# Optimization experiments

Hardware: AMD Instinct MI355X
Metric: run time of the kernel (lower is better)

Reference implementation:

```python
import jax, jax.numpy as jnp
import numpy as np

N = 50000      # nodes
E = 800000     # edges (avg degree 16)
CIN = 64       # in_channels
COUT = 128     # hidden_channels (block out_channels)
TC = 512       # time_channels = 4*hidden
H = 4          # attention heads
DH = COUT // H # head dim
G = 8          # group-norm groups
SLOPE = 0.01   # LeakyReLU default slope


def group_norm(x, w, b, groups=G, eps=1e-5):
    n, c = x.shape
    xg = x.reshape(n, groups, c // groups)
    mu = xg.mean(-1, keepdims=True)
    var = xg.var(-1, keepdims=True)
    xn = ((xg - mu) * jax.lax.rsqrt(var + eps)).reshape(n, c)
    return xn * w + b


def gcn_conv(x, W, b, row, col, ew, n):
    # GCNConv: add self loops (weight 1), symmetric normalization
    sl = jnp.arange(n)
    r = jnp.concatenate([row, sl])
    c = jnp.concatenate([col, sl])
    w2 = jnp.concatenate([ew, jnp.ones((n,), ew.dtype)])
    deg = jax.ops.segment_sum(w2, c, num_segments=n)
    dinv = jnp.where(deg > 0, jax.lax.rsqrt(deg), 0.0)
    norm = dinv[r] * w2 * dinv[c]            # [E+N]
    xw = x @ W                                # [N, Cout]
    out = jax.ops.segment_sum(norm[:, None] * xw[r], c, num_segments=n)
    return out + b


def gat_conv(x, Wa, a_src, a_dst, a_edge, ba, row, col, ew, n):
    # GAT-style attention conv; self-loop edge weight filled with max(edge_weight)
    sl = jnp.arange(n)
    fill = ew.max()
    r = jnp.concatenate([row, sl])
    c = jnp.concatenate([col, sl])
    w2 = jnp.concatenate([ew, jnp.full((n,), fill, ew.dtype)])
    h = (x @ Wa).reshape(n, H, DH)            # [N, H, DH]
    al_s = (h * a_src).sum(-1)                # [N, H]
    al_d = (h * a_dst).sum(-1)                # [N, H]
    logits = jax.nn.leaky_relu(al_s[r] + al_d[c] + a_edge * w2[:, None], 0.2)
    m = jax.ops.segment_max(logits, c, num_segments=n)
    e = jnp.exp(logits - m[c])
    s = jax.ops.segment_sum(e, c, num_segments=n)
    alpha = e / (s[c] + 1e-16)                # [E+N, H]
    out = jax.ops.segment_sum(alpha[:, :, None] * h[r], c, num_segments=n)
    return out.reshape(n, H * DH) + ba


def setup_inputs() -> dict:
    key = jax.random.key(0)
    ks = jax.random.split(key, 24)
    def w(k, shape, fan_in):
        return (jax.random.normal(k, shape, jnp.float32) / np.sqrt(fan_in)).astype(jnp.float32)
    inp = {
        "x": jax.random.normal(ks[0], (N, CIN), jnp.float32),
        "t": jax.random.normal(ks[1], (TC,), jnp.float32),
        "edge_index": jax.random.randint(ks[2], (2, E), 0, N, jnp.int32),
        "edge_weight": jax.random.uniform(ks[3], (E,), jnp.float32),
        # ResBlock norm/conv params
        "gn0_w": jnp.ones((CIN,), jnp.float32), "gn0_b": jnp.zeros((CIN,), jnp.float32),
        "W1": w(ks[4], (CIN, COUT), CIN), "b1": jnp.zeros((COUT,), jnp.float32),
        "gn1_w": jnp.ones((COUT,), jnp.float32), "gn1_b": jnp.zeros((COUT,), jnp.float32),
        "W2": w(ks[5], (COUT, COUT), COUT), "b2": jnp.zeros((COUT,), jnp.float32),
        "Wres": w(ks[6], (CIN, COUT), CIN),
        "te_w": w(ks[7], (TC, COUT), TC), "te_b": jnp.zeros((COUT,), jnp.float32),
        # AttnBlock params
        "gn2_w": jnp.ones((COUT,), jnp.float32), "gn2_b": jnp.zeros((COUT,), jnp.float32),
        "Wa": w(ks[8], (COUT, H * DH), COUT),
        "a_src": w(ks[9], (H, DH), DH), "a_dst": w(ks[10], (H, DH), DH),
        "a_edge": w(ks[11], (H,), 1), "ba": jnp.zeros((H * DH,), jnp.float32),
    }
    return inp


def reference(x, t, edge_index, edge_weight,
              gn0_w, gn0_b, W1, b1, gn1_w, gn1_b, W2, b2, Wres, te_w, te_b,
              gn2_w, gn2_b, Wa, a_src, a_dst, a_edge, ba):
    row, col = edge_index[0], edge_index[1]
    leaky = lambda z: jax.nn.leaky_relu(z, SLOPE)
    # ResBlock (n_layers=2)
    h = gcn_conv(leaky(group_norm(x, gn0_w, gn0_b)), W1, b1, row, col, edge_weight, N)
    tt = leaky(t) @ te_w + te_b               # time embed, broadcasts over nodes
    h = h + tt
    h = gcn_conv(leaky(group_norm(h, gn1_w, gn1_b)), W2, b2, row, col, edge_weight, N)
    h = h + x @ Wres                          # residual (Cin != Cout -> Linear)
    # AttnBlock (n_layers=1)
    a = leaky(group_norm(h, gn2_w, gn2_b))
    out = gat_conv(a, Wa, a_src, a_dst, a_edge, ba, row, col, edge_weight, N)
    return out
```

## Files before the change

kernel.cpp:

```cpp
#include <hip/hip_runtime.h>
#include <math.h>

#define ELLW 48
#define CH 4096

typedef __attribute__((ext_vector_type(8))) short frag_ab;
typedef __attribute__((ext_vector_type(4))) float frag_cd;

__device__ __forceinline__ float lk(float v, float s) { return v > 0.f ? v : v * s; }
__device__ __forceinline__ unsigned short f2b(float f) {
    unsigned u = __float_as_uint(f);
    return (unsigned short)((u + 0x7fffu + ((u >> 16) & 1u)) >> 16);
}
__device__ __forceinline__ float b2f(unsigned h) { return __uint_as_float(h << 16); }

__global__ __launch_bounds__(256) void k_bhist(const int* __restrict__ col,
                                               int* __restrict__ bhist, int E, int NB) {
    __shared__ int lh[256];
    int tid = threadIdx.x;
    if (tid < NB) lh[tid] = 0;
    __syncthreads();
    int base = blockIdx.x * CH;
#pragma unroll
    for (int i = 0; i < CH / 256; ++i) {
        int e = base + i * 256 + tid;
        if (e < E) atomicAdd(&lh[col[e] >> 8], 1);
    }
    __syncthreads();
    if (tid < NB && lh[tid]) atomicAdd(&bhist[tid], lh[tid]);
}

__global__ __launch_bounds__(256) void k_bscan(const int* __restrict__ bhist,
                                               int* __restrict__ boff,
                                               int* __restrict__ cursor, int NB, int E) {
    __shared__ int s[256];
    int tid = threadIdx.x;
    int v = (tid < NB) ? bhist[tid] : 0;
    s[tid] = v; __syncthreads();
#pragma unroll
    for (int d = 1; d < 256; d <<= 1) {
        int t = (tid >= d) ? s[tid - d] : 0;
        __syncthreads();
        s[tid] += t;
        __syncthreads();
    }
    if (tid < NB) { int o = s[tid] - v; boff[tid] = o; cursor[tid] = o; }
    if (tid == 0) boff[NB] = E;
}

__global__ __launch_bounds__(256) void k_bscatter(const int* __restrict__ row,
                                                  const int* __restrict__ col,
                                                  const float* __restrict__ ew,
                                                  int* __restrict__ cursor,
                                                  uint2* __restrict__ stage,
                                                  float* __restrict__ bmax, int E, int NB) {
    __shared__ int lh[256];
    __shared__ int lbase[256];
    constexpr int PT = CH / 256;
    int tid = threadIdx.x;
    if (tid < NB) lh[tid] = 0;
    __syncthreads();
    int base = blockIdx.x * CH;
    unsigned entry[PT]; int cc[PT]; int lpos[PT]; bool val[PT];
    float m = 0.f;
#pragma unroll
    for (int i = 0; i < PT; ++i) {
        int e = base + i * 256 + tid;
        val[i] = (e < E);
        entry[i] = 0; cc[i] = 0; lpos[i] = 0;
        if (val[i]) {
            int r = row[e], c = col[e];
            float w = ew[e];
            m = fmaxf(m, w);
            entry[i] = (unsigned)r | ((unsigned)f2b(w) << 16);
            cc[i] = c;
            lpos[i] = atomicAdd(&lh[c >> 8], 1);
        }
    }
    __syncthreads();
    if (tid < NB) lbase[tid] = lh[tid] ? atomicAdd(&cursor[tid], lh[tid]) : 0;
    __syncthreads();
#pragma unroll
    for (int i = 0; i < PT; ++i) {
        if (val[i]) {
            int b = cc[i] >> 8;
            stage[lbase[b] + lpos[i]] = make_uint2(entry[i], (unsigned)(cc[i] & 255));
        }
    }
    for (int o = 32; o; o >>= 1) m = fmaxf(m, __shfl_down(m, o, 64));
    __shared__ float sm[4];
    if ((tid & 63) == 0) sm[tid >> 6] = m;
    __syncthreads();
    if (tid == 0) bmax[blockIdx.x] = fmaxf(fmaxf(sm[0], sm[1]), fmaxf(sm[2], sm[3]));
}

__global__ __launch_bounds__(256) void k_bbuild(const int* __restrict__ boff,
                                                const uint2* __restrict__ stage,
                                                unsigned* __restrict__ ell,
                                                int* __restrict__ cnt,
                                                float* __restrict__ dinv, int n) {
    __shared__ unsigned tile[256 * ELLW];
    __shared__ int lcnt[256];
    int tid = threadIdx.x;
    int bk = blockIdx.x;
    lcnt[tid] = 0;
    __syncthreads();
    int s = boff[bk], e2 = boff[bk + 1];
    for (int i = s + tid; i < e2; i += 256) {
        uint2 p = stage[i];
        int c8 = p.y;
        int pos = atomicAdd(&lcnt[c8], 1);
        if (pos < ELLW) tile[c8 * ELLW + pos] = p.x;
    }
    __syncthreads();
    int node = bk * 256 + tid;
    if (node >= n) return;
    int c = min(lcnt[tid], ELLW);
    cnt[node] = c;
    float sw = 1.f;
    for (int j = 0; j < c; ++j) sw += b2f(tile[tid * ELLW + j] >> 16);
    dinv[node] = rsqrtf(sw);
    unsigned* dst = ell + (size_t)node * ELLW;
#pragma unroll
    for (int j = 0; j < ELLW / 4; ++j)
        *(uint4*)(dst + j * 4) = *(uint4*)(tile + tid * ELLW + j * 4);
}

template <int K>
__device__ __forceinline__ void repack1(const float* __restrict__ W,
                                        unsigned short* __restrict__ Wp, int i) {
    int k = i >> 7, nn = i & 127;
    int kc = k >> 5, quad = (k >> 3) & 3, j = k & 7;
    Wp[(((size_t)(kc * 4 + quad) * 128) + nn) * 8 + j] = f2b(W[i]);
}

__global__ __launch_bounds__(256) void k_prep(const float* __restrict__ t,
                                              const float* __restrict__ te_w,
                                              const float* __restrict__ te_b,
                                              const float* __restrict__ b1,
                                              float* __restrict__ tt,
                                              const float* __restrict__ bmax,
                                              float* __restrict__ fill, int nbm,
                                              const float* __restrict__ W1,
                                              const float* __restrict__ W2,
                                              const float* __restrict__ Wa,
                                              const float* __restrict__ Wres,
                                              unsigned short* W1p, unsigned short* W2p,
                                              unsigned short* Wap, unsigned short* Wrp) {
    int tid = threadIdx.x;
    int blk = blockIdx.x;
    if (blk == 0) {
        if (tid < 128) {
            float s = te_b[tid] + b1[tid];
            for (int k = 0; k < 512; ++k) {
                float tv = t[k]; tv = tv > 0.f ? tv : 0.01f * tv;
                s = fmaf(tv, te_w[k * 128 + tid], s);
            }
            tt[tid] = s;
        }
    } else if (blk == 1) {
        float m = 0.f;
        for (int i = tid; i < nbm; i += 256) m = fmaxf(m, bmax[i]);
        for (int o = 32; o; o >>= 1) m = fmaxf(m, __shfl_down(m, o, 64));
        __shared__ float sm[4];
        if ((tid & 63) == 0) sm[tid >> 6] = m;
        __syncthreads();
        if (tid == 0) *fill = fmaxf(fmaxf(sm[0], sm[1]), fmaxf(sm[2], sm[3]));
    } else {
        int i = (blk - 2) * 256 + tid;
        if (i < 8192)        repack1<64>(W1, W1p, i);
        else if (i < 24576)  repack1<128>(W2, W2p, i - 8192);
        else if (i < 40960)  repack1<128>(Wa, Wap, i - 24576);
        else if (i < 49152)  repack1<64>(Wres, Wrp, i - 40960);
    }
}

__global__ __launch_bounds__(256) void k_mgemm1(const float* __restrict__ X,
                                                const float* __restrict__ gw,
                                                const float* __restrict__ gb,
                                                const unsigned short* __restrict__ Wp,
                                                unsigned short* __restrict__ OUTh,
                                                unsigned short* __restrict__ xh,
                                                const float* __restrict__ dinv, int n) {
    int tid = threadIdx.x;
    int wave = tid >> 6, lane = tid & 63;
    int quad = lane >> 4, l16 = lane & 15;
    int rbase = blockIdx.x * 64 + wave * 16;
    int arow = rbase + l16; if (arow >= n) arow = n - 1;
    frag_ab afrag[2];
    const float* xr = X + (size_t)arow * 64 + quad * 8;
#pragma unroll
    for (int kc = 0; kc < 2; ++kc) {
        float4 u0 = *(const float4*)(xr + kc * 32);
        float4 u1 = *(const float4*)(xr + kc * 32 + 4);
        float v[8] = {u0.x, u0.y, u0.z, u0.w, u1.x, u1.y, u1.z, u1.w};
        float s = 0.f, sq = 0.f;
#pragma unroll
        for (int j = 0; j < 8; ++j) { s += v[j]; sq = fmaf(v[j], v[j], sq); }
        float mu = s * 0.125f;
        float var = sq * 0.125f - mu * mu;
        float rstd = rsqrtf(var + 1e-5f);
        const float* wj = gw + kc * 32 + quad * 8;
        const float* bj = gb + kc * 32 + quad * 8;
        unsigned pk[4], pr[4];
#pragma unroll
        for (int j = 0; j < 8; j += 2) {
            float y0 = lk((v[j + 0] - mu) * rstd * wj[j + 0] + bj[j + 0], 0.01f);
            float y1 = lk((v[j + 1] - mu) * rstd * wj[j + 1] + bj[j + 1], 0.01f);
            pk[j / 2] = (unsigned)f2b(y0) | ((unsigned)f2b(y1) << 16);
            pr[j / 2] = (unsigned)f2b(v[j]) | ((unsigned)f2b(v[j + 1]) << 16);
        }
        afrag[kc] = *(frag_ab*)pk;
        *(uint4*)(xh + (size_t)arow * 64 + kc * 32 + quad * 8) = *(uint4*)pr;
    }
    frag_cd acc[8];
#pragma unroll
    for (int t = 0; t < 8; ++t) acc[t] = (frag_cd){0.f, 0.f, 0.f, 0.f};
#pragma unroll
    for (int kc = 0; kc < 2; ++kc) {
        const unsigned short* bp = Wp + ((size_t)(kc * 4 + quad) * 128 + l16) * 8;
#pragma unroll
        for (int t = 0; t < 8; ++t) {
            frag_ab b = *(const frag_ab*)(bp + (size_t)t * 128);
            acc[t] = __builtin_amdgcn_mfma_f32_16x16x32_bf16(afrag[kc], b, acc[t], 0, 0, 0);
        }
    }
#pragma unroll
    for (int reg = 0; reg < 4; ++reg) {
        int r = rbase + quad * 4 + reg;
        if (r >= n) continue;
        float sc = dinv[r];
#pragma unroll
        for (int t = 0; t < 8; ++t)
            OUTh[(size_t)r * 128 + t * 16 + l16] = f2b(sc * acc[t][reg]);
    }
}

__global__ __launch_bounds__(256) void k_mgemm2(const unsigned short* __restrict__ X1,
                                                const unsigned short* __restrict__ W2p,
                                                const unsigned short* __restrict__ X2,
                                                const unsigned short* __restrict__ Wrp,
                                                unsigned short* __restrict__ OUTh,
                                                float* __restrict__ C2,
                                                const float* __restrict__ bias,
                                                const float* __restrict__ dinv, int n) {
    int tid = threadIdx.x;
    int wave = tid >> 6, lane = tid & 63;
    int quad = lane >> 4, l16 = lane & 15;
    int rbase = blockIdx.x * 64 + wave * 16;
    int arow = rbase + l16; if (arow >= n) arow = n - 1;
    frag_cd acc1[8], acc2[8];
#pragma unroll
    for (int t = 0; t < 8; ++t) {
        acc1[t] = (frag_cd){0.f, 0.f, 0.f, 0.f};
        acc2[t] = (frag_cd){0.f, 0.f, 0.f, 0.f};
    }
    const unsigned short* ap1 = X1 + (size_t)arow * 128 + quad * 8;
#pragma unroll
    for (int kc = 0; kc < 4; ++kc) {
        frag_ab a = *(const frag_ab*)(ap1 + kc * 32);
        const unsigned short* bp = W2p + ((size_t)(kc * 4 + quad) * 128 + l16) * 8;
#pragma unroll
        for (int t = 0; t < 8; ++t) {
            frag_ab b = *(const frag_ab*)(bp + (size_t)t * 128);
            acc1[t] = __builtin_amdgcn_mfma_f32_16x16x32_bf16(a, b, acc1[t], 0, 0, 0);
        }
    }
    const unsigned short* ap2 = X2 + (size_t)arow * 64 + quad * 8;
#pragma unroll
    for (int kc = 0; kc < 2; ++kc) {
        frag_ab a = *(const frag_ab*)(ap2 + kc * 32);
        const unsigned short* bp = Wrp + ((size_t)(kc * 4 + quad) * 128 + l16) * 8;
#pragma unroll
        for (int t = 0; t < 8; ++t) {
            frag_ab b = *(const frag_ab*)(bp + (size_t)t * 128);
            acc2[t] = __builtin_amdgcn_mfma_f32_16x16x32_bf16(a, b, acc2[t], 0, 0, 0);
        }
    }
#pragma unroll
    for (int reg = 0; reg < 4; ++reg) {
        int r = rbase + quad * 4 + reg;
        if (r >= n) continue;
        float sc = dinv[r];
#pragma unroll
        for (int t = 0; t < 8; ++t) {
            int c = t * 16 + l16;
            size_t o = (size_t)r * 128 + c;
            OUTh[o] = f2b(sc * acc1[t][reg]);
            C2[o] = bias[c] + acc2[t][reg];
        }
    }
}

__global__ __launch_bounds__(256) void k_mgemmA(const unsigned short* __restrict__ Xh,
                                                const unsigned short* __restrict__ Wp,
                                                unsigned short* __restrict__ OUTh,
                                                const float* __restrict__ a_src,
                                                const float* __restrict__ a_dst,
                                                float* __restrict__ als,
                                                float* __restrict__ ald, int n) {
    int tid = threadIdx.x;
    int wave = tid >> 6, lane = tid & 63;
    int quad = lane >> 4, l16 = lane & 15;
    int rbase = blockIdx.x * 64 + wave * 16;
    int arow = rbase + l16; if (arow >= n) arow = n - 1;
    frag_cd acc[8];
#pragma unroll
    for (int t = 0; t < 8; ++t) acc[t] = (frag_cd){0.f, 0.f, 0.f, 0.f};
    const unsigned short* ap = Xh + (size_t)arow * 128 + quad * 8;
#pragma unroll
    for (int kc = 0; kc < 4; ++kc) {
        frag_ab a = *(const frag_ab*)(ap + kc * 32);
        const unsigned short* bp = Wp + ((size_t)(kc * 4 + quad) * 128 + l16) * 8;
#pragma unroll
        for (int t = 0; t < 8; ++t) {
            frag_ab b = *(const frag_ab*)(bp + (size_t)t * 128);
            acc[t] = __builtin_amdgcn_mfma_f32_16x16x32_bf16(a, b, acc[t], 0, 0, 0);
        }
    }
#pragma unroll
    for (int reg = 0; reg < 4; ++reg) {
        int r = rbase + quad * 4 + reg;
        if (r >= n) continue;
#pragma unroll
        for (int t = 0; t < 8; ++t)
            OUTh[(size_t)r * 128 + t * 16 + l16] = f2b(acc[t][reg]);
    }
    float ps[4][4], pd[4][4];
#pragma unroll
    for (int hd = 0; hd < 4; ++hd) {
        float slo = a_src[hd * 32 + l16], shi = a_src[hd * 32 + 16 + l16];
        float dlo = a_dst[hd * 32 + l16], dhi = a_dst[hd * 32 + 16 + l16];
#pragma unroll
        for (int reg = 0; reg < 4; ++reg) {
            ps[reg][hd] = fmaf(acc[2 * hd][reg], slo, acc[2 * hd + 1][reg] * shi);
            pd[reg][hd] = fmaf(acc[2 * hd][reg], dlo, acc[2 * hd + 1][reg] * dhi);
        }
    }
#pragma unroll
    for (int m = 1; m < 16; m <<= 1) {
#pragma unroll
        for (int reg = 0; reg < 4; ++reg)
#pragma unroll
            for (int hd = 0; hd < 4; ++hd) {
                ps[reg][hd] += __shfl_xor(ps[reg][hd], m, 64);
                pd[reg][hd] += __shfl_xor(pd[reg][hd], m, 64);
            }
    }
    if (l16 == 0) {
#pragma unroll
        for (int reg = 0; reg < 4; ++reg) {
            int r = rbase + quad * 4 + reg;
            if (r >= n) continue;
#pragma unroll
            for (int hd = 0; hd < 4; ++hd) {
                als[r * 4 + hd] = ps[reg][hd];
                ald[r * 4 + hd] = pd[reg][hd];
            }
        }
    }
}

template <int BASEVEC>
__global__ __launch_bounds__(256) void k_gather_gn(const int* __restrict__ cnt,
                                                   const unsigned* __restrict__ ell,
                                                   const float* __restrict__ dinv,
                                                   const unsigned short* __restrict__ Bh,
                                                   const float* __restrict__ basevec,
                                                   const float* __restrict__ basebuf,
                                                   const float* __restrict__ gw,
                                                   const float* __restrict__ gb,
                                                   unsigned short* __restrict__ outh, int n) {
    int gid = blockIdx.x * 256 + threadIdx.x;
    int node = gid >> 5, q = gid & 31;
    if (node >= n) return;
    int s = node * ELLW;
    int e2 = s + min(cnt[node], ELLW);
    float a0 = 0.f, a1 = 0.f, a2 = 0.f, a3 = 0.f;
    int j = s;
    for (; j + 4 <= e2; j += 4) {
        uint4 pe = *(const uint4*)(ell + j);
        int r0 = pe.x & 0xffffu, r1 = pe.y & 0xffffu, r2 = pe.z & 0xffffu, r3 = pe.w & 0xffffu;
        float w0 = b2f(pe.x >> 16), w1 = b2f(pe.y >> 16);
        float w2 = b2f(pe.z >> 16), w3 = b2f(pe.w >> 16);
        uint2 v0 = *(const uint2*)(Bh + (size_t)r0 * 128 + q * 4);
        uint2 v1 = *(const uint2*)(Bh + (size_t)r1 * 128 + q * 4);
        uint2 v2 = *(const uint2*)(Bh + (size_t)r2 * 128 + q * 4);
        uint2 v3 = *(const uint2*)(Bh + (size_t)r3 * 128 + q * 4);
        a0 = fmaf(w0, b2f(v0.x & 0xffffu), a0); a1 = fmaf(w0, b2f(v0.x >> 16), a1);
        a2 = fmaf(w0, b2f(v0.y & 0xffffu), a2); a3 = fmaf(w0, b2f(v0.y >> 16), a3);
        a0 = fmaf(w1, b2f(v1.x & 0xffffu), a0); a1 = fmaf(w1, b2f(v1.x >> 16), a1);
        a2 = fmaf(w1, b2f(v1.y & 0xffffu), a2); a3 = fmaf(w1, b2f(v1.y >> 16), a3);
        a0 = fmaf(w2, b2f(v2.x & 0xffffu), a0); a1 = fmaf(w2, b2f(v2.x >> 16), a1);
        a2 = fmaf(w2, b2f(v2.y & 0xffffu), a2); a3 = fmaf(w2, b2f(v2.y >> 16), a3);
        a0 = fmaf(w3, b2f(v3.x & 0xffffu), a0); a1 = fmaf(w3, b2f(v3.x >> 16), a1);
        a2 = fmaf(w3, b2f(v3.y & 0xffffu), a2); a3 = fmaf(w3, b2f(v3.y >> 16), a3);
    }
    for (; j < e2; ++j) {
        unsigned pe = ell[j];
        int r = pe & 0xffffu;
        float nw = b2f(pe >> 16);
        uint2 hv = *(const uint2*)(Bh + (size_t)r * 128 + q * 4);
        a0 = fmaf(nw, b2f(hv.x & 0xffffu), a0);
        a1 = fmaf(nw, b2f(hv.x >> 16), a1);
        a2 = fmaf(nw, b2f(hv.y & 0xffffu), a2);
        a3 = fmaf(nw, b2f(hv.y >> 16), a3);
    }
    float dc = dinv[node];
    uint2 sv = *(const uint2*)(Bh + (size_t)node * 128 + q * 4);
    a0 = dc * (a0 + b2f(sv.x & 0xffffu));
    a1 = dc * (a1 + b2f(sv.x >> 16));
    a2 = dc * (a2 + b2f(sv.y & 0xffffu));
    a3 = dc * (a3 + b2f(sv.y >> 16));
    float h0, h1, h2, h3;
    if constexpr (BASEVEC) {
        float4 bb = *(const float4*)(basevec + q * 4);
        h0 = bb.x + a0; h1 = bb.y + a1; h2 = bb.z + a2; h3 = bb.w + a3;
    } else {
        float4 bb = *(const float4*)(basebuf + (size_t)node * 128 + q * 4);
        h0 = bb.x + a0; h1 = bb.y + a1; h2 = bb.z + a2; h3 = bb.w + a3;
    }
    float sum = (h0 + h1) + (h2 + h3);
    float sq = fmaf(h0, h0, fmaf(h1, h1, fmaf(h2, h2, h3 * h3)));
    sum += __shfl_xor(sum, 1, 64); sum += __shfl_xor(sum, 2, 64);
    sq  += __shfl_xor(sq, 1, 64);  sq  += __shfl_xor(sq, 2, 64);
    float mu = sum * (1.0f / 16.0f);
    float var = sq * (1.0f / 16.0f) - mu * mu;
    float rstd = rsqrtf(var + 1e-5f);
    float4 gwv = *(const float4*)(gw + q * 4);
    float4 gbv = *(const float4*)(gb + q * 4);
    float y0 = lk((h0 - mu) * rstd * gwv.x + gbv.x, 0.01f);
    float y1 = lk((h1 - mu) * rstd * gwv.y + gbv.y, 0.01f);
    float y2 = lk((h2 - mu) * rstd * gwv.z + gbv.z, 0.01f);
    float y3 = lk((h3 - mu) * rstd * gwv.w + gbv.w, 0.01f);
    uint2 o;
    o.x = (unsigned)f2b(y0) | ((unsigned)f2b(y1) << 16);
    o.y = (unsigned)f2b(y2) | ((unsigned)f2b(y3) << 16);
    *(uint2*)(outh + (size_t)node * 128 + q * 4) = o;
}

__global__ __launch_bounds__(256) void k_gat_gather(const int* __restrict__ cnt,
                                                    const unsigned* __restrict__ ell,
                                                    const float* __restrict__ als,
                                                    const float* __restrict__ ald,
                                                    const float* __restrict__ a_edge,
                                                    const float* __restrict__ fill,
                                                    const unsigned short* __restrict__ HAh,
                                                    const float* __restrict__ ba,
                                                    float* __restrict__ out, int n) {
    int gid = blockIdx.x * 256 + threadIdx.x;
    int node = gid >> 5, q = gid & 31, hd = q >> 3;
    if (node >= n) return;
    int s = node * ELLW;
    int e2 = s + min(cnt[node], ELLW);
    float ae = a_edge[hd];
    float aldc = ald[node * 4 + hd];
    float wself = *fill;
    float pself = __expf(lk(als[node * 4 + hd] + aldc + ae * wself, 0.2f));
    float den = pself;
    uint2 hv = *(const uint2*)(HAh + (size_t)node * 128 + q * 4);
    float a0 = pself * b2f(hv.x & 0xffffu), a1 = pself * b2f(hv.x >> 16);
    float a2 = pself * b2f(hv.y & 0xffffu), a3 = pself * b2f(hv.y >> 16);
    int j = s;
    for (; j + 4 <= e2; j += 4) {
        uint4 pe = *(const uint4*)(ell + j);
        int r0 = pe.x & 0xffffu, r1 = pe.y & 0xffffu, r2 = pe.z & 0xffffu, r3 = pe.w & 0xffffu;
        float w0 = b2f(pe.x >> 16), w1 = b2f(pe.y >> 16);
        float w2 = b2f(pe.z >> 16), w3 = b2f(pe.w >> 16);
        float s0 = als[r0 * 4 + hd], s1 = als[r1 * 4 + hd];
        float s2 = als[r2 * 4 + hd], s3 = als[r3 * 4 + hd];
        uint2 v0 = *(const uint2*)(HAh + (size_t)r0 * 128 + q * 4);
        uint2 v1 = *(const uint2*)(HAh + (size_t)r1 * 128 + q * 4);
        uint2 v2 = *(const uint2*)(HAh + (size_t)r2 * 128 + q * 4);
        uint2 v3 = *(const uint2*)(HAh + (size_t)r3 * 128 + q * 4);
        float pe0 = __expf(lk(s0 + aldc + ae * w0, 0.2f));
        float pe1 = __expf(lk(s1 + aldc + ae * w1, 0.2f));
        float pe2 = __expf(lk(s2 + aldc + ae * w2, 0.2f));
        float pe3 = __expf(lk(s3 + aldc + ae * w3, 0.2f));
        den += (pe0 + pe1) + (pe2 + pe3);
        a0 = fmaf(pe0, b2f(v0.x & 0xffffu), a0); a1 = fmaf(pe0, b2f(v0.x >> 16), a1);
        a2 = fmaf(pe0, b2f(v0.y & 0xffffu), a2); a3 = fmaf(pe0, b2f(v0.y >> 16), a3);
        a0 = fmaf(pe1, b2f(v1.x & 0xffffu), a0); a1 = fmaf(pe1, b2f(v1.x >> 16), a1);
        a2 = fmaf(pe1, b2f(v1.y & 0xffffu), a2); a3 = fmaf(pe1, b2f(v1.y >> 16), a3);
        a0 = fmaf(pe2, b2f(v2.x & 0xffffu), a0); a1 = fmaf(pe2, b2f(v2.x >> 16), a1);
        a2 = fmaf(pe2, b2f(v2.y & 0xffffu), a2); a3 = fmaf(pe2, b2f(v2.y >> 16), a3);
        a0 = fmaf(pe3, b2f(v3.x & 0xffffu), a0); a1 = fmaf(pe3, b2f(v3.x >> 16), a1);
        a2 = fmaf(pe3, b2f(v3.y & 0xffffu), a2); a3 = fmaf(pe3, b2f(v3.y >> 16), a3);
    }
    for (; j < e2; ++j) {
        unsigned pe = ell[j];
        int r = pe & 0xffffu;
        float w = b2f(pe >> 16);
        float pev = __expf(lk(als[r * 4 + hd] + aldc + ae * w, 0.2f));
        den += pev;
        uint2 v = *(const uint2*)(HAh + (size_t)r * 128 + q * 4);
        a0 = fmaf(pev, b2f(v.x & 0xffffu), a0);
        a1 = fmaf(pev, b2f(v.x >> 16), a1);
        a2 = fmaf(pev, b2f(v.y & 0xffffu), a2);
        a3 = fmaf(pev, b2f(v.y >> 16), a3);
    }
    float inv = 1.0f / (den + 1e-16f);
    const float* bb = ba + q * 4;
    float4 o;
    o.x = bb[0] + a0 * inv; o.y = bb[1] + a1 * inv;
    o.z = bb[2] + a2 * inv; o.w = bb[3] + a3 * inv;
    *(float4*)&out[(size_t)node * 128 + q * 4] = o;
}

extern "C" void kernel_launch(void* const* d_in, const int* in_sizes, int n_in,
                              void* d_out, int out_size, void* d_ws, size_t ws_size,
                              hipStream_t stream) {
    const float* x     = (const float*)d_in[0];
    const float* t     = (const float*)d_in[1];
    const int*   eidx  = (const int*)d_in[2];
    const float* ew    = (const float*)d_in[3];
    const float* gn0_w = (const float*)d_in[4];
    const float* gn0_b = (const float*)d_in[5];
    const float* W1    = (const float*)d_in[6];
    const float* b1    = (const float*)d_in[7];
    const float* gn1_w = (const float*)d_in[8];
    const float* gn1_b = (const float*)d_in[9];
    const float* W2    = (const float*)d_in[10];
    const float* b2    = (const float*)d_in[11];
    const float* Wres  = (const float*)d_in[12];
    const float* te_w  = (const float*)d_in[13];
    const float* te_b  = (const float*)d_in[14];
    const float* gn2_w = (const float*)d_in[15];
    const float* gn2_b = (const float*)d_in[16];
    const float* Wa    = (const float*)d_in[17];
    const float* a_src = (const float*)d_in[18];
    const float* a_dst = (const float*)d_in[19];
    const float* a_edge= (const float*)d_in[20];
    const float* ba    = (const float*)d_in[21];

    int n = in_sizes[0] / 64;
    int E = in_sizes[3];
    const int* rowp = eidx;
    const int* colp = eidx + E;
    int NB = (n + 255) >> 8;

    char* p = (char*)d_ws;
    float* fC = (float*)p;                 p += (size_t)n * 128 * 4;
    unsigned short* fDh = (unsigned short*)p; p += (size_t)n * 128 * 2;
    unsigned short* fBh = (unsigned short*)p; p += (size_t)n * 128 * 2;
    unsigned short* xh  = (unsigned short*)p; p += (size_t)n * 64 * 2;
    unsigned* ell = (unsigned*)p;          p += (size_t)n * ELLW * 4;
    uint2* stage = (uint2*)p;              p += (size_t)E * 8;
    unsigned short* W1p   = (unsigned short*)p; p += 64 * 128 * 2;
    unsigned short* W2p   = (unsigned short*)p; p += 128 * 128 * 2;
    unsigned short* Wap   = (unsigned short*)p; p += 128 * 128 * 2;
    unsigned short* Wresp = (unsigned short*)p; p += 64 * 128 * 2;
    float* dinv = (float*)p;               p += (size_t)n * 4;
    float* tt  = (float*)p;                p += 128 * 4;
    float* fill = (float*)p;               p += 16;
    float* als = (float*)p;                p += (size_t)4 * n * 4;
    float* ald = (float*)p;                p += (size_t)4 * n * 4;
    int* cnt    = (int*)p;                 p += (size_t)n * 4;
    int* bhist  = (int*)p;                 p += 256 * 4;
    int* boff   = (int*)p;                 p += 260 * 4;
    int* cursor = (int*)p;                 p += 256 * 4;
    float* bmax = (float*)p;               p += 4096 * 4;
    float* out = (float*)d_out;

    auto cdiv = [](long long a, long long b) { return (int)((a + b - 1) / b); };
    int gridE = cdiv(E, CH);

    hipMemsetAsync(bhist, 0, NB * 4, stream);
    k_bhist<<<gridE, 256, 0, stream>>>(colp, bhist, E, NB);
    k_bscan<<<1, 256, 0, stream>>>(bhist, boff, cursor, NB, E);
    k_bscatter<<<gridE, 256, 0, stream>>>(rowp, colp, ew, cursor, stage, bmax, E, NB);
    k_bbuild<<<NB, 256, 0, stream>>>(boff, stage, ell, cnt, dinv, n);
    k_prep<<<194, 256, 0, stream>>>(t, te_w, te_b, b1, tt, bmax, fill, gridE,
                                    W1, W2, Wa, Wres, W1p, W2p, Wap, Wresp);

    k_mgemm1<<<cdiv(n, 64), 256, 0, stream>>>(x, gn0_w, gn0_b, W1p, fBh, xh, dinv, n);
    k_gather_gn<1><<<cdiv(32LL * n, 256), 256, 0, stream>>>(cnt, ell, dinv, fBh, tt, nullptr,
                                                            gn1_w, gn1_b, fDh, n);

    k_mgemm2<<<cdiv(n, 64), 256, 0, stream>>>(fDh, W2p, xh, Wresp, fBh, fC, b2, dinv, n);
    k_gather_gn<0><<<cdiv(32LL * n, 256), 256, 0, stream>>>(cnt, ell, dinv, fBh, nullptr, fC,
                                                            gn2_w, gn2_b, fDh, n);

    k_mgemmA<<<cdiv(n, 64), 256, 0, stream>>>(fDh, Wap, fBh, a_src, a_dst, als, ald, n);
    k_gat_gather<<<cdiv(32LL * n, 256), 256, 0, stream>>>(cnt, ell, als, ald, a_edge, fill, fBh, ba, out, n);
}
```

Baseline: 322.7 us.

## Merge graph-prep launches and unroll gather loops to eight edges

Removes the memset and the separate prep kernel. The histogram kernel now writes per-block partial counts, which the scan sums, and it also does the time-embedding and weight-repack work. The fill-max reduction moves into block 0 of the ELL build kernel. Separately, both the GCN and GAT gather loops now issue eight neighbour loads before consuming them, to expose more memory-level parallelism, at the cost of more registers. Block 0 of the build kernel calls __syncthreads inside a branch, but that branch is uniform across the block.

```diff
diff --git a/kernel.cpp b/kernel.cpp
--- a/kernel.cpp
+++ b/kernel.cpp
@@ -14,34 +14,79 @@
 }
 __device__ __forceinline__ float b2f(unsigned h) { return __uint_as_float(h << 16); }
 
-__global__ __launch_bounds__(256) void k_bhist(const int* __restrict__ col,
-                                               int* __restrict__ bhist, int E, int NB) {
-    __shared__ int lh[256];
+template <int K>
+__device__ __forceinline__ void repack1(const float* __restrict__ W,
+                                        unsigned short* __restrict__ Wp, int i) {
+    int k = i >> 7, nn = i & 127;
+    int kc = k >> 5, quad = (k >> 3) & 3, j = k & 7;
+    Wp[(((size_t)(kc * 4 + quad) * 128) + nn) * 8 + j] = f2b(W[i]);
+}
+
+__global__ __launch_bounds__(256) void k_phase1(const int* __restrict__ col,
+                                                int* __restrict__ part, int E, int gridE,
+                                                const float* __restrict__ t,
+                                                const float* __restrict__ te_w,
+                                                const float* __restrict__ te_b,
+                                                const float* __restrict__ b1,
+                                                float* __restrict__ tt,
+                                                const float* __restrict__ W1,
+                                                const float* __restrict__ W2,
+                                                const float* __restrict__ Wa,
+                                                const float* __restrict__ Wres,
+                                                unsigned short* W1p, unsigned short* W2p,
+                                                unsigned short* Wap, unsigned short* Wrp) {
     int tid = threadIdx.x;
-    if (tid < NB) lh[tid] = 0;
-    __syncthreads();
-    int base = blockIdx.x * CH;
-#pragma unroll
-    for (int i = 0; i < CH / 256; ++i) {
-        int e = base + i * 256 + tid;
-        if (e < E) atomicAdd(&lh[col[e] >> 8], 1);
-    }
-    __syncthreads();
-    if (tid < NB && lh[tid]) atomicAdd(&bhist[tid], lh[tid]);
-}
-
-__global__ __launch_bounds__(256) void k_bscan(const int* __restrict__ bhist,
+    int blk = blockIdx.x;
+    if (blk < gridE) {
+        __shared__ int lh[256];
+        lh[tid] = 0;
+        __syncthreads();
+        int base = blk * CH;
+#pragma unroll
+        for (int i = 0; i < CH / 256; ++i) {
+            int e = base + i * 256 + tid;
+            if (e < E) atomicAdd(&lh[col[e] >> 8], 1);
+        }
+        __syncthreads();
+        part[blk * 256 + tid] = lh[tid];
+    } else if (blk == gridE) {
+        if (tid < 128) {
+            float s = te_b[tid] + b1[tid];
+            for (int k = 0; k < 512; ++k) {
+                float tv = t[k]; tv = tv > 0.f ? tv : 0.01f * tv;
+                s = fmaf(tv, te_w[k * 128 + tid], s);
+            }
+            tt[tid] = s;
+        }
+    } else {
+        int i = (blk - gridE - 1) * 256 + tid;
+        if (i < 8192)        repack1<64>(W1, W1p, i);
+        else if (i < 24576)  repack1<128>(W2, W2p, i - 8192);
+        else if (i < 40960)  repack1<128>(Wa, Wap, i - 24576);
+        else if (i < 49152)  repack1<64>(Wres, Wrp, i - 40960);
+    }
+}
+
+__global__ __launch_bounds__(256) void k_bscan(const int* __restrict__ part,
                                                int* __restrict__ boff,
-                                               int* __restrict__ cursor, int NB, int E) {
+                                               int* __restrict__ cursor,
+                                               int NB, int E, int gridE) {
     __shared__ int s[256];
     int tid = threadIdx.x;
-    int v = (tid < NB) ? bhist[tid] : 0;
+    int acc[8] = {0, 0, 0, 0, 0, 0, 0, 0};
+    int g = 0;
+    for (; g + 8 <= gridE; g += 8)
+#pragma unroll
+        for (int k = 0; k < 8; ++k) acc[k] += part[(g + k) * 256 + tid];
+    int v = ((acc[0] + acc[1]) + (acc[2] + acc[3])) + ((acc[4] + acc[5]) + (acc[6] + acc[7]));
+    for (; g < gridE; ++g) v += part[g * 256 + tid];
+    if (tid >= NB) v = 0;
     s[tid] = v; __syncthreads();
 #pragma unroll
     for (int d = 1; d < 256; d <<= 1) {
-        int t = (tid >= d) ? s[tid - d] : 0;
+        int tv = (tid >= d) ? s[tid - d] : 0;
         __syncthreads();
-        s[tid] += t;
+        s[tid] += tv;
         __syncthreads();
     }
     if (tid < NB) { int o = s[tid] - v; boff[tid] = o; cursor[tid] = o; }
@@ -98,13 +143,24 @@
                                                 const uint2* __restrict__ stage,
                                                 unsigned* __restrict__ ell,
                                                 int* __restrict__ cnt,
-                                                float* __restrict__ dinv, int n) {
+                                                float* __restrict__ dinv,
+                                                const float* __restrict__ bmax,
+                                                float* __restrict__ fill, int n, int nbm) {
     __shared__ unsigned tile[256 * ELLW];
     __shared__ int lcnt[256];
     int tid = threadIdx.x;
     int bk = blockIdx.x;
     lcnt[tid] = 0;
     __syncthreads();
+    if (bk == 0) {
+        float m = 0.f;
+        for (int i = tid; i < nbm; i += 256) m = fmaxf(m, bmax[i]);
+        for (int o = 32; o; o >>= 1) m = fmaxf(m, __shfl_down(m, o, 64));
+        __shared__ float sm[4];
+        if ((tid & 63) == 0) sm[tid >> 6] = m;
+        __syncthreads();
+        if (tid == 0) *fill = fmaxf(fmaxf(sm[0], sm[1]), fmaxf(sm[2], sm[3]));
+    }
     int s = boff[bk], e2 = boff[bk + 1];
     for (int i = s + tid; i < e2; i += 256) {
         uint2 p = stage[i];
@@ -124,55 +180,6 @@
 #pragma unroll
     for (int j = 0; j < ELLW / 4; ++j)
         *(uint4*)(dst + j * 4) = *(uint4*)(tile + tid * ELLW + j * 4);
-}
-
-template <int K>
-__device__ __forceinline__ void repack1(const float* __restrict__ W,
-                                        unsigned short* __restrict__ Wp, int i) {
-    int k = i >> 7, nn = i & 127;
-    int kc = k >> 5, quad = (k >> 3) & 3, j = k & 7;
-    Wp[(((size_t)(kc * 4 + quad) * 128) + nn) * 8 + j] = f2b(W[i]);
-}
-
-__global__ __launch_bounds__(256) void k_prep(const float* __restrict__ t,
-                                              const float* __restrict__ te_w,
-                                              const float* __restrict__ te_b,
-                                              const float* __restrict__ b1,
-                                              float* __restrict__ tt,
-                                              const float* __restrict__ bmax,
-                                              float* __restrict__ fill, int nbm,
-                                              const float* __restrict__ W1,
-                                              const float* __restrict__ W2,
-                                              const float* __restrict__ Wa,
-                                              const float* __restrict__ Wres,
-                                              unsigned short* W1p, unsigned short* W2p,
-                                              unsigned short* Wap, unsigned short* Wrp) {
-    int tid = threadIdx.x;
-    int blk = blockIdx.x;
-    if (blk == 0) {
-        if (tid < 128) {
-            float s = te_b[tid] + b1[tid];
-            for (int k = 0; k < 512; ++k) {
-                float tv = t[k]; tv = tv > 0.f ? tv : 0.01f * tv;
-                s = fmaf(tv, te_w[k * 128 + tid], s);
-            }
-            tt[tid] = s;
-        }
-    } else if (blk == 1) {
-        float m = 0.f;
-        for (int i = tid; i < nbm; i += 256) m = fmaxf(m, bmax[i]);
-        for (int o = 32; o; o >>= 1) m = fmaxf(m, __shfl_down(m, o, 64));
-        __shared__ float sm[4];
-        if ((tid & 63) == 0) sm[tid >> 6] = m;
-        __syncthreads();
-        if (tid == 0) *fill = fmaxf(fmaxf(sm[0], sm[1]), fmaxf(sm[2], sm[3]));
-    } else {
-        int i = (blk - 2) * 256 + tid;
-        if (i < 8192)        repack1<64>(W1, W1p, i);
-        else if (i < 24576)  repack1<128>(W2, W2p, i - 8192);
-        else if (i < 40960)  repack1<128>(Wa, Wap, i - 24576);
-        else if (i < 49152)  repack1<64>(Wres, Wrp, i - 40960);
-    }
 }
 
 __global__ __launch_bounds__(256) void k_mgemm1(const float* __restrict__ X,
@@ -378,29 +385,44 @@
     int e2 = s + min(cnt[node], ELLW);
     float a0 = 0.f, a1 = 0.f, a2 = 0.f, a3 = 0.f;
     int j = s;
-    for (; j + 4 <= e2; j += 4) {
-        uint4 pe = *(const uint4*)(ell + j);
-        int r0 = pe.x & 0xffffu, r1 = pe.y & 0xffffu, r2 = pe.z & 0xffffu, r3 = pe.w & 0xffffu;
-        float w0 = b2f(pe.x >> 16), w1 = b2f(pe.y >> 16);
-        float w2 = b2f(pe.z >> 16), w3 = b2f(pe.w >> 16);
-        uint2 v0 = *(const uint2*)(Bh + (size_t)r0 * 128 + q * 4);
-        uint2 v1 = *(const uint2*)(Bh + (size_t)r1 * 128 + q * 4);
-        uint2 v2 = *(const uint2*)(Bh + (size_t)r2 * 128 + q * 4);
-        uint2 v3 = *(const uint2*)(Bh + (size_t)r3 * 128 + q * 4);
-        a0 = fmaf(w0, b2f(v0.x & 0xffffu), a0); a1 = fmaf(w0, b2f(v0.x >> 16), a1);
-        a2 = fmaf(w0, b2f(v0.y & 0xffffu), a2); a3 = fmaf(w0, b2f(v0.y >> 16), a3);
-        a0 = fmaf(w1, b2f(v1.x & 0xffffu), a0); a1 = fmaf(w1, b2f(v1.x >> 16), a1);
-        a2 = fmaf(w1, b2f(v1.y & 0xffffu), a2); a3 = fmaf(w1, b2f(v1.y >> 16), a3);
-        a0 = fmaf(w2, b2f(v2.x & 0xffffu), a0); a1 = fmaf(w2, b2f(v2.x >> 16), a1);
-        a2 = fmaf(w2, b2f(v2.y & 0xffffu), a2); a3 = fmaf(w2, b2f(v2.y >> 16), a3);
-        a0 = fmaf(w3, b2f(v3.x & 0xffffu), a0); a1 = fmaf(w3, b2f(v3.x >> 16), a1);
-        a2 = fmaf(w3, b2f(v3.y & 0xffffu), a2); a3 = fmaf(w3, b2f(v3.y >> 16), a3);
+    for (; j + 8 <= e2; j += 8) {
+        uint4 pa = *(const uint4*)(ell + j);
+        uint4 pb = *(const uint4*)(ell + j + 4);
+        unsigned pe[8] = {pa.x, pa.y, pa.z, pa.w, pb.x, pb.y, pb.z, pb.w};
+        uint2 v[8];
+#pragma unroll
+        for (int k = 0; k < 8; ++k)
+            v[k] = *(const uint2*)(Bh + (size_t)(pe[k] & 0xffffu) * 128 + q * 4);
+#pragma unroll
+        for (int k = 0; k < 8; ++k) {
+            float w = b2f(pe[k] >> 16);
+            a0 = fmaf(w, b2f(v[k].x & 0xffffu), a0);
+            a1 = fmaf(w, b2f(v[k].x >> 16), a1);
+            a2 = fmaf(w, b2f(v[k].y & 0xffffu), a2);
+            a3 = fmaf(w, b2f(v[k].y >> 16), a3);
+        }
+    }
+    if (j + 4 <= e2) {
+        uint4 pa = *(const uint4*)(ell + j);
+        unsigned pe[4] = {pa.x, pa.y, pa.z, pa.w};
+        uint2 v[4];
+#pragma unroll
+        for (int k = 0; k < 4; ++k)
+            v[k] = *(const uint2*)(Bh + (size_t)(pe[k] & 0xffffu) * 128 + q * 4);
+#pragma unroll
+        for (int k = 0; k < 4; ++k) {
+            float w = b2f(pe[k] >> 16);
+            a0 = fmaf(w, b2f(v[k].x & 0xffffu), a0);
+            a1 = fmaf(w, b2f(v[k].x >> 16), a1);
+            a2 = fmaf(w, b2f(v[k].y & 0xffffu), a2);
+            a3 = fmaf(w, b2f(v[k].y >> 16), a3);
+        }
+        j += 4;
     }
     for (; j < e2; ++j) {
         unsigned pe = ell[j];
-        int r = pe & 0xffffu;
         float nw = b2f(pe >> 16);
-        uint2 hv = *(const uint2*)(Bh + (size_t)r * 128 + q * 4);
+        uint2 hv = *(const uint2*)(Bh + (size_t)(pe & 0xffffu) * 128 + q * 4);
         a0 = fmaf(nw, b2f(hv.x & 0xffffu), a0);
         a1 = fmaf(nw, b2f(hv.x >> 16), a1);
         a2 = fmaf(nw, b2f(hv.y & 0xffffu), a2);
@@ -462,36 +484,52 @@
     float a0 = pself * b2f(hv.x & 0xffffu), a1 = pself * b2f(hv.x >> 16);
     float a2 = pself * b2f(hv.y & 0xffffu), a3 = pself * b2f(hv.y >> 16);
     int j = s;
-    for (; j + 4 <= e2; j += 4) {
-        uint4 pe = *(const uint4*)(ell + j);
-        int r0 = pe.x & 0xffffu, r1 = pe.y & 0xffffu, r2 = pe.z & 0xffffu, r3 = pe.w & 0xffffu;
-        float w0 = b2f(pe.x >> 16), w1 = b2f(pe.y >> 16);
-        float w2 = b2f(pe.z >> 16), w3 = b2f(pe.w >> 16);
-        float s0 = als[r0 * 4 + hd], s1 = als[r1 * 4 + hd];
-        float s2 = als[r2 * 4 + hd], s3 = als[r3 * 4 + hd];
-        uint2 v0 = *(const uint2*)(HAh + (size_t)r0 * 128 + q * 4);
-        uint2 v1 = *(const uint2*)(HAh + (size_t)r1 * 128 + q * 4);
-        uint2 v2 = *(const uint2*)(HAh + (size_t)r2 * 128 + q * 4);
-        uint2 v3 = *(const uint2*)(HAh + (size_t)r3 * 128 + q * 4);
-        float pe0 = __expf(lk(s0 + aldc + ae * w0, 0.2f));
-        float pe1 = __expf(lk(s1 + aldc + ae * w1, 0.2f));
-        float pe2 = __expf(lk(s2 + aldc + ae * w2, 0.2f));
-        float pe3 = __expf(lk(s3 + aldc + ae * w3, 0.2f));
-        den += (pe0 + pe1) + (pe2 + pe3);
-        a0 = fmaf(pe0, b2f(v0.x & 0xffffu), a0); a1 = fmaf(pe0, b2f(v0.x >> 16), a1);
-        a2 = fmaf(pe0, b2f(v0.y & 0xffffu), a2); a3 = fmaf(pe0, b2f(v0.y >> 16), a3);
-        a0 = fmaf(pe1, b2f(v1.x & 0xffffu), a0); a1 = fmaf(pe1, b2f(v1.x >> 16), a1);
-        a2 = fmaf(pe1, b2f(v1.y & 0xffffu), a2); a3 = fmaf(pe1, b2f(v1.y >> 16), a3);
-        a0 = fmaf(pe2, b2f(v2.x & 0xffffu), a0); a1 = fmaf(pe2, b2f(v2.x >> 16), a1);
-        a2 = fmaf(pe2, b2f(v2.y & 0xffffu), a2); a3 = fmaf(pe2, b2f(v2.y >> 16), a3);
-        a0 = fmaf(pe3, b2f(v3.x & 0xffffu), a0); a1 = fmaf(pe3, b2f(v3.x >> 16), a1);
-        a2 = fmaf(pe3, b2f(v3.y & 0xffffu), a2); a3 = fmaf(pe3, b2f(v3.y >> 16), a3);
+    for (; j + 8 <= e2; j += 8) {
+        uint4 pa = *(const uint4*)(ell + j);
+        uint4 pb = *(const uint4*)(ell + j + 4);
+        unsigned pe[8] = {pa.x, pa.y, pa.z, pa.w, pb.x, pb.y, pb.z, pb.w};
+        float sl[8]; uint2 v[8];
+#pragma unroll
+        for (int k = 0; k < 8; ++k) {
+            int r = pe[k] & 0xffffu;
+            sl[k] = als[r * 4 + hd];
+            v[k] = *(const uint2*)(HAh + (size_t)r * 128 + q * 4);
+        }
+#pragma unroll
+        for (int k = 0; k < 8; ++k) {
+            float pev = __expf(lk(sl[k] + aldc + ae * b2f(pe[k] >> 16), 0.2f));
+            den += pev;
+            a0 = fmaf(pev, b2f(v[k].x & 0xffffu), a0);
+            a1 = fmaf(pev, b2f(v[k].x >> 16), a1);
+            a2 = fmaf(pev, b2f(v[k].y & 0xffffu), a2);
+            a3 = fmaf(pev, b2f(v[k].y >> 16), a3);
+        }
+    }
+    if (j + 4 <= e2) {
+        uint4 pa = *(const uint4*)(ell + j);
+        unsigned pe[4] = {pa.x, pa.y, pa.z, pa.w};
+        float sl[4]; uint2 v[4];
+#pragma unroll
+        for (int k = 0; k < 4; ++k) {
+            int r = pe[k] & 0xffffu;
+            sl[k] = als[r * 4 + hd];
+            v[k] = *(const uint2*)(HAh + (size_t)r * 128 + q * 4);
+        }
+#pragma unroll
+        for (int k = 0; k < 4; ++k) {
+            float pev = __expf(lk(sl[k] + aldc + ae * b2f(pe[k] >> 16), 0.2f));
+            den += pev;
+            a0 = fmaf(pev, b2f(v[k].x & 0xffffu), a0);
+            a1 = fmaf(pev, b2f(v[k].x >> 16), a1);
+            a2 = fmaf(pev, b2f(v[k].y & 0xffffu), a2);
+            a3 = fmaf(pev, b2f(v[k].y >> 16), a3);
+        }
+        j += 4;
     }
     for (; j < e2; ++j) {
         unsigned pe = ell[j];
         int r = pe & 0xffffu;
-        float w = b2f(pe >> 16);
-        float pev = __expf(lk(als[r * 4 + hd] + aldc + ae * w, 0.2f));
+        float pev = __expf(lk(als[r * 4 + hd] + aldc + ae * b2f(pe >> 16), 0.2f));
         den += pev;
         uint2 v = *(const uint2*)(HAh + (size_t)r * 128 + q * 4);
         a0 = fmaf(pev, b2f(v.x & 0xffffu), a0);
@@ -539,6 +577,9 @@
     const int* colp = eidx + E;
     int NB = (n + 255) >> 8;
 
+    auto cdiv = [](long long a, long long b) { return (int)((a + b - 1) / b); };
+    int gridE = cdiv(E, CH);
+
     char* p = (char*)d_ws;
     float* fC = (float*)p;                 p += (size_t)n * 128 * 4;
     unsigned short* fDh = (unsigned short*)p; p += (size_t)n * 128 * 2;
@@ -556,22 +597,18 @@
     float* als = (float*)p;                p += (size_t)4 * n * 4;
     float* ald = (float*)p;                p += (size_t)4 * n * 4;
     int* cnt    = (int*)p;                 p += (size_t)n * 4;
-    int* bhist  = (int*)p;                 p += 256 * 4;
+    int* part   = (int*)p;                 p += (size_t)gridE * 256 * 4;
     int* boff   = (int*)p;                 p += 260 * 4;
     int* cursor = (int*)p;                 p += 256 * 4;
     float* bmax = (float*)p;               p += 4096 * 4;
     float* out = (float*)d_out;
 
-    auto cdiv = [](long long a, long long b) { return (int)((a + b - 1) / b); };
-    int gridE = cdiv(E, CH);
-
-    hipMemsetAsync(bhist, 0, NB * 4, stream);
-    k_bhist<<<gridE, 256, 0, stream>>>(colp, bhist, E, NB);
-    k_bscan<<<1, 256, 0, stream>>>(bhist, boff, cursor, NB, E);
+    k_phase1<<<gridE + 1 + 192, 256, 0, stream>>>(colp, part, E, gridE,
+                                                  t, te_w, te_b, b1, tt,
+                                                  W1, W2, Wa, Wres, W1p, W2p, Wap, Wresp);
+    k_bscan<<<1, 256, 0, stream>>>(part, boff, cursor, NB, E, gridE);
     k_bscatter<<<gridE, 256, 0, stream>>>(rowp, colp, ew, cursor, stage, bmax, E, NB);
-    k_bbuild<<<NB, 256, 0, stream>>>(boff, stage, ell, cnt, dinv, n);
-    k_prep<<<194, 256, 0, stream>>>(t, te_w, te_b, b1, tt, bmax, fill, gridE,
-                                    W1, W2, Wa, Wres, W1p, W2p, Wap, Wresp);
+    k_bbuild<<<NB, 256, 0, stream>>>(boff, stage, ell, cnt, dinv, bmax, fill, n, gridE);
 
     k_mgemm1<<<cdiv(n, 64), 256, 0, stream>>>(x, gn0_w, gn0_b, W1p, fBh, xh, dinv, n);
     k_gather_gn<1><<<cdiv(32LL * n, 256), 256, 0, stream>>>(cnt, ell, dinv, fBh, tt, nullptr,
```

Result: faster. 311.4 us (-3.5%).
